# Optimization experiments

Hardware: AMD Instinct MI355X
Metric: run time of the kernel (lower is better)

The kernel has to match this reference:

```python
import jax, jax.numpy as jnp
import numpy as np

N = 25000   # nodes of type 'window'
E = 200000  # edges per relation
H = 512     # hidden_channels
OUT = 250   # out_channels
L = 4       # num_layers
R = 3       # relations: near, close, sim


def setup_inputs() -> dict:
    key = jax.random.key(0)
    ks = jax.random.split(key, 8)
    s = 1.0 / np.sqrt(H).astype(np.float32)
    x = jax.random.normal(ks[0], (N, H), jnp.float32)
    W_pre = jax.random.normal(ks[1], (H, H), jnp.float32) * s
    W_post = jax.random.normal(ks[2], (H, H), jnp.float32) * s
    Wl = jax.random.normal(ks[3], (L, R, H, H), jnp.float32) * s   # SAGEConv lin_l (neighbors)
    Wr = jax.random.normal(ks[4], (L, R, H, H), jnp.float32) * s   # SAGEConv lin_r (root)
    bl = jnp.zeros((L, R, H), jnp.float32)                         # lin_l bias
    W_out = jax.random.normal(ks[5], (H, OUT), jnp.float32) * s
    b_out = jnp.zeros((OUT,), jnp.float32)
    edges = jax.random.randint(ks[6], (R, 2, E), 0, N, jnp.int32)  # [rel, (src,dst), E]
    return dict(x=x, W_pre=W_pre, W_post=W_post, Wl=Wl, Wr=Wr, bl=bl,
                W_out=W_out, b_out=b_out, edges=edges)


def _leaky(v):
    return jnp.where(v >= 0, v, 0.2 * v)


def reference(x, W_pre, W_post, Wl, Wr, bl, W_out, b_out, edges):
    # pretransform + post_transform: leaky(leaky(x @ Wpre) @ Wpost)
    h = _leaky(_leaky(x @ W_pre) @ W_post)

    # per-relation destination in-degree (constant across layers)
    inv_deg = []
    for r in range(R):
        cnt = jax.ops.segment_sum(jnp.ones((E,), h.dtype), edges[r, 1], num_segments=N)
        inv_deg.append(1.0 / jnp.maximum(cnt, 1.0))  # [N]

    for l in range(L):
        acc = jnp.zeros_like(h)
        for r in range(R):
            src, dst = edges[r, 0], edges[r, 1]
            # mean aggregation of neighbor features over destinations
            agg = jax.ops.segment_sum(h[src], dst, num_segments=N) * inv_deg[r][:, None]
            # SAGEConv: lin_l(agg) + lin_r(x_root)
            acc = acc + (agg @ Wl[l, r] + bl[l, r] + h @ Wr[l, r])
        # HeteroConv aggr='mean' across relations, then LeakyReLU(0.2)
        h = _leaky(acc / R)

    return h @ W_out + b_out
```

## Files before the change

kernel.cpp:

```cpp
#include <hip/hip_runtime.h>

#define N_ 25000
#define E_ 200000
#define H_ 512
#define OUT_ 250
#define WSZ (H_ * H_)

typedef unsigned short u16;
typedef unsigned int u32;
typedef __bf16 bf16x8 __attribute__((ext_vector_type(8)));
typedef float f32x4 __attribute__((ext_vector_type(4)));

__device__ __forceinline__ u16 f2b(float f) {
  union { float f; u32 u; } c; c.f = f;
  u32 r = c.u + 0x7FFFu + ((c.u >> 16) & 1u);
  return (u16)(r >> 16);
}
__device__ __forceinline__ void async16(const void* g, void* l) {
  __builtin_amdgcn_global_load_lds((__attribute__((address_space(1))) void*)g,
                                   (__attribute__((address_space(3))) void*)l, 16, 0, 0);
}

__global__ void conv_x(const float* __restrict__ x, u16* __restrict__ xb, int n4) {
  int i = blockIdx.x * 256 + threadIdx.x;
  if (i >= n4) return;
  const float4 v = *(const float4*)(x + (size_t)i * 4);
  ushort4 o;
  o.x = f2b(v.x); o.y = f2b(v.y); o.z = f2b(v.z); o.w = f2b(v.w);
  *(ushort4*)(xb + (size_t)i * 4) = o;
}

__global__ void prep_wt(const float* __restrict__ Wpre, const float* __restrict__ Wpost,
                        const float* __restrict__ Wl, const float* __restrict__ Wr,
                        u16* __restrict__ WT) {
  __shared__ u16 tile[32][33];
  const int id = blockIdx.z;
  const int tx = blockIdx.x, ty = blockIdx.y;
  const int x = threadIdx.x, y = threadIdx.y;
  const float* src = nullptr;
  bool sum3 = false;
  if (id == 0) src = Wpre;
  else if (id == 1) src = Wpost;
  else {
    int li = (id - 2) >> 2, ri = (id - 2) & 3;
    if (ri < 3) src = Wl + (size_t)(li * 3 + ri) * WSZ;
    else { sum3 = true; src = Wr + (size_t)(li * 3) * WSZ; }
  }
#pragma unroll
  for (int i = 0; i < 4; ++i) {
    int row = ty * 32 + y + i * 8;
    int col = tx * 32 + x;
    float f = src[(size_t)row * 512 + col];
    if (sum3) f += src[WSZ + (size_t)row * 512 + col] + src[2 * WSZ + (size_t)row * 512 + col];
    tile[y + i * 8][x] = f2b(f);
  }
  __syncthreads();
#pragma unroll
  for (int i = 0; i < 4; ++i) {
    WT[(size_t)id * WSZ + (tx * 32 + y + i * 8) * 512 + ty * 32 + x] = tile[x][y + i * 8];
  }
}

__global__ void prep_wout(const float* __restrict__ Wout, u16* __restrict__ WoutT) {
  __shared__ u16 tile[32][33];
  const int tx = blockIdx.x, ty = blockIdx.y;
  const int x = threadIdx.x, y = threadIdx.y;
#pragma unroll
  for (int i = 0; i < 4; ++i) {
    int row = ty * 32 + y + i * 8;
    int col = tx * 32 + x;
    tile[y + i * 8][x] = (col < OUT_) ? f2b(Wout[(size_t)row * OUT_ + col]) : (u16)0;
  }
  __syncthreads();
#pragma unroll
  for (int i = 0; i < 4; ++i) {
    WoutT[(tx * 32 + y + i * 8) * 512 + ty * 32 + x] = tile[x][y + i * 8];
  }
}

__global__ void prep_bias(const float* __restrict__ bl, const float* __restrict__ bout,
                          float* __restrict__ blSum, float* __restrict__ bOutF) {
  int t = threadIdx.x;
  for (int l = 0; l < 4; ++l)
    blSum[l * 512 + t] = bl[(l * 3 + 0) * 512 + t] + bl[(l * 3 + 1) * 512 + t] +
                         bl[(l * 3 + 2) * 512 + t];
  if (t < 256) bOutF[t] = (t < OUT_) ? bout[t] : 0.0f;
}

__global__ void hist_kernel(const int* __restrict__ edges, int* __restrict__ counts) {
  int idx = blockIdx.x * 256 + threadIdx.x;
  if (idx >= 3 * E_) return;
  int r = idx / E_, e = idx - r * E_;
  int dst = edges[r * 2 * E_ + E_ + e];
  atomicAdd(&counts[r * N_ + dst], 1);
}

__global__ __launch_bounds__(1024) void scan_kernel(const int* __restrict__ counts,
                                                    int* __restrict__ rowptr,
                                                    int* __restrict__ cursor) {
  const int r = blockIdx.x;
  const int* cnt = counts + r * N_;
  int* rp = rowptr + r * (N_ + 1);
  int* cur = cursor + r * N_;
  __shared__ int wsum[2][16];
  const int tid = threadIdx.x;
  const int wv = tid >> 6, lane = tid & 63;
  int roff = 0;
  int par = 0;
  for (int base = 0; base < N_; base += 1024, par ^= 1) {
    int v = (base + tid < N_) ? cnt[base + tid] : 0;
    int inc = v;
#pragma unroll
    for (int d = 1; d < 64; d <<= 1) {
      int t = __shfl_up(inc, d, 64);
      if (lane >= d) inc += t;
    }
    if (lane == 63) wsum[par][wv] = inc;
    __syncthreads();
    if (tid < 16) {
      int s = wsum[par][tid];
#pragma unroll
      for (int d = 1; d < 16; d <<= 1) {
        int t = __shfl_up(s, d, 64);
        if (tid >= d) s += t;
      }
      wsum[par][tid] = s;
    }
    __syncthreads();
    int woff = (wv == 0) ? 0 : wsum[par][wv - 1];
    int excl = roff + woff + inc - v;
    if (base + tid < N_) { rp[base + tid] = excl; cur[base + tid] = excl; }
    roff += wsum[par][15];
  }
  if (tid == 0) rp[N_] = roff;
}

__global__ void scatter_kernel(const int* __restrict__ edges, int* __restrict__ cursor,
                               int* __restrict__ colidx) {
  int idx = blockIdx.x * 256 + threadIdx.x;
  if (idx >= 3 * E_) return;
  int r = idx / E_, e = idx - r * E_;
  int src = edges[r * 2 * E_ + e];
  int dst = edges[r * 2 * E_ + E_ + e];
  int pos = atomicAdd(&cursor[r * N_ + dst], 1);
  colidx[r * E_ + pos] = src;
}

__global__ void invdeg_kernel(const int* __restrict__ counts, float* __restrict__ invdeg) {
  int idx = blockIdx.x * 256 + threadIdx.x;
  if (idx >= 3 * N_) return;
  invdeg[idx] = 1.0f / fmaxf((float)counts[idx], 1.0f);
}

__device__ __forceinline__ void acc8(float* acc, uint4 u) {
  union { u32 u; float f; } c;
  c.u = u.x << 16;          acc[0] += c.f;
  c.u = u.x & 0xffff0000u;  acc[1] += c.f;
  c.u = u.y << 16;          acc[2] += c.f;
  c.u = u.y & 0xffff0000u;  acc[3] += c.f;
  c.u = u.z << 16;          acc[4] += c.f;
  c.u = u.z & 0xffff0000u;  acc[5] += c.f;
  c.u = u.w << 16;          acc[6] += c.f;
  c.u = u.w & 0xffff0000u;  acc[7] += c.f;
}

__global__ __launch_bounds__(256) void agg_kernel(const u16* __restrict__ h,
                                                  const int* __restrict__ rowptr,
                                                  const int* __restrict__ colidx,
                                                  const float* __restrict__ invdeg,
                                                  u16* __restrict__ agg) {
  const int chunk = blockIdx.x & 7;
  const int nb = blockIdx.x >> 3;
  const int r = blockIdx.y;
  const int wv = threadIdx.x >> 6;
  const int lane = threadIdx.x & 63;
  const int grp = lane >> 3, sub = lane & 7;
  const int node = nb * 32 + wv * 8 + grp;
  if (node >= N_) return;
  const int* rp = rowptr + r * (N_ + 1);
  const int* ci = colidx + r * E_;
  const u16* hb = h + chunk * 64 + sub * 8;
  const int s = rp[node], e = rp[node + 1];
  float acc[8] = {0.f, 0.f, 0.f, 0.f, 0.f, 0.f, 0.f, 0.f};
  int p = s;
  if (p < e) {
    int src = ci[p];
    uint4 u = *(const uint4*)(hb + (size_t)src * 512);
    for (++p; p < e; ++p) {
      int src2 = ci[p];
      uint4 u2 = *(const uint4*)(hb + (size_t)src2 * 512);
      acc8(acc, u);
      u = u2;
    }
    acc8(acc, u);
  }
  const float sc = invdeg[r * N_ + node];
  uint4 o;
  o.x = (u32)f2b(acc[0] * sc) | ((u32)f2b(acc[1] * sc) << 16);
  o.y = (u32)f2b(acc[2] * sc) | ((u32)f2b(acc[3] * sc) << 16);
  o.z = (u32)f2b(acc[4] * sc) | ((u32)f2b(acc[5] * sc) << 16);
  o.w = (u32)f2b(acc[6] * sc) | ((u32)f2b(acc[7] * sc) << 16);
  *(uint4*)(agg + ((size_t)r * N_ + node) * 512 + chunk * 64 + sub * 8) = o;
}

#define BM 128
#define BN 128
#define BK 64
__global__ __launch_bounds__(256, 4) void gemm_mfma(
    const u16* __restrict__ A0, const u16* __restrict__ A1,
    const u16* __restrict__ A2, const u16* __restrict__ A3,
    const u16* __restrict__ Bt, const float* __restrict__ bias,
    u16* __restrict__ C, float* __restrict__ Cf,
    int M, int G, int ldc, int Nreal, float scale, int leaky) {
  __shared__ __align__(16) u16 As[BM * BK];
  __shared__ __align__(16) u16 Bs[BN * BK];
  const int tid = threadIdx.x;
  const int lane = tid & 63;
  const int w = tid >> 6;

  const int gx = gridDim.x;
  const int lin = blockIdx.y * gx + blockIdx.x;
  const int gsz = gx * 8;
  const int grp = lin / gsz;
  const int l = lin - grp * gsz;
  const int rem = (int)gridDim.y - grp * 8;
  int by, bx;
  if (rem >= 8) { by = grp * 8 + (l & 7); bx = l >> 3; }
  else          { by = grp * 8 + l % rem; bx = l / rem; }
  const int row0 = by * BM;
  const int col0 = bx * BN;

  int aOff[4], bOff[4], lOff[4];
#pragma unroll
  for (int i = 0; i < 4; ++i) {
    const int idx = i * 256 + tid;
    const int arow = idx >> 3;
    const int c = (idx & 7) ^ (arow & 7);
    int grow = row0 + arow; if (grow >= M) grow = M - 1;
    aOff[i] = grow * 512 + c * 8;
    bOff[i] = (col0 + arow) * 512 + c * 8;
    lOff[i] = idx * 16;
  }

  const int lm = lane & 15;
  const int lk = lane >> 4;
  const int x0 = ((lk ^ (lane & 7)) << 3);
  const int x1 = (((4 + lk) ^ (lane & 7)) << 3);
  const int wm = (w >> 1) * 64;
  const int wn = (w & 1) * 64;
  int aRow[4], bRow[4];
#pragma unroll
  for (int i = 0; i < 4; ++i) {
    aRow[i] = (wm + i * 16 + lm) * BK;
    bRow[i] = (wn + i * 16 + lm) * BK;
  }

  f32x4 acc[4][4] = {};

  for (int g = 0; g < G; ++g) {
    const u16* Ag = (g == 0) ? A0 : (g == 1) ? A1 : (g == 2) ? A2 : A3;
    const u16* Bg = Bt + ((size_t)g << 18);
#pragma unroll
    for (int ki = 0; ki < 8; ++ki) {
      const u16* Ab = Ag + ki * 64;
      const u16* Bb = Bg + ki * 64;
#pragma unroll
      for (int i = 0; i < 4; ++i) {
        async16(Ab + aOff[i], (char*)As + lOff[i]);
        async16(Bb + bOff[i], (char*)Bs + lOff[i]);
      }
      __syncthreads();
      {
        bf16x8 af[4], bfr[4];
#pragma unroll
        for (int i = 0; i < 4; ++i) {
          af[i]  = *(const bf16x8*)((const char*)As + ((aRow[i] + x0) << 1));
          bfr[i] = *(const bf16x8*)((const char*)Bs + ((bRow[i] + x0) << 1));
        }
#pragma unroll
        for (int i = 0; i < 4; ++i)
#pragma unroll
          for (int j = 0; j < 4; ++j)
            acc[i][j] = __builtin_amdgcn_mfma_f32_16x16x32_bf16(af[i], bfr[j], acc[i][j], 0, 0, 0);
#pragma unroll
        for (int i = 0; i < 4; ++i) {
          af[i]  = *(const bf16x8*)((const char*)As + ((aRow[i] + x1) << 1));
          bfr[i] = *(const bf16x8*)((const char*)Bs + ((bRow[i] + x1) << 1));
        }
#pragma unroll
        for (int i = 0; i < 4; ++i)
#pragma unroll
          for (int j = 0; j < 4; ++j)
            acc[i][j] = __builtin_amdgcn_mfma_f32_16x16x32_bf16(af[i], bfr[j], acc[i][j], 0, 0, 0);
      }
      __syncthreads();
    }
  }

  const int crow_base = row0 + wm + (lk << 2);
  const int ccol_base = col0 + wn + lm;
#pragma unroll
  for (int i = 0; i < 4; ++i) {
#pragma unroll
    for (int j = 0; j < 4; ++j) {
      const int ccol = ccol_base + j * 16;
      const float badd = bias ? bias[ccol] : 0.0f;
#pragma unroll
      for (int rg = 0; rg < 4; ++rg) {
        const int crow = crow_base + i * 16 + rg;
        if (crow < M && ccol < Nreal) {
          float v = (acc[i][j][rg] + badd) * scale;
          if (leaky) v = (v >= 0.0f) ? v : 0.2f * v;
          if (Cf) Cf[(size_t)crow * ldc + ccol] = v;
          else    C[(size_t)crow * ldc + ccol] = f2b(v);
        }
      }
    }
  }
}

extern "C" void kernel_launch(void* const* d_in, const int* in_sizes, int n_in,
                              void* d_out, int out_size, void* d_ws, size_t ws_size,
                              hipStream_t stream) {
  const float* x     = (const float*)d_in[0];
  const float* Wpre  = (const float*)d_in[1];
  const float* Wpost = (const float*)d_in[2];
  const float* Wl    = (const float*)d_in[3];
  const float* Wr    = (const float*)d_in[4];
  const float* bl    = (const float*)d_in[5];
  const float* Wout  = (const float*)d_in[6];
  const float* bout  = (const float*)d_in[7];
  const int*   edges = (const int*)d_in[8];
  float* out = (float*)d_out;

  char* p = (char*)d_ws;
  auto alloc = [&](size_t b) { void* q = (void*)p; p += (b + 255) & ~(size_t)255; return q; };
  u16*   WT     = (u16*)alloc((size_t)18 * WSZ * 2);
  u16*   WoutT  = (u16*)alloc((size_t)256 * 512 * 2);
  float* blSum  = (float*)alloc(4 * 512 * 4);
  float* bOutF  = (float*)alloc(256 * 4);
  u16*   hA     = (u16*)alloc((size_t)N_ * 512 * 2);
  u16*   hB     = (u16*)alloc((size_t)N_ * 512 * 2);
  u16*   aggb   = (u16*)alloc((size_t)3 * N_ * 512 * 2);
  int*   counts = (int*)alloc(3 * N_ * 4);
  float* invdeg = (float*)alloc(3 * N_ * 4);
  int*   rowptr = (int*)alloc(3 * (N_ + 1) * 4);
  int*   cursor = (int*)alloc(3 * N_ * 4);
  int*   colidx = (int*)alloc((size_t)3 * E_ * 4);
  u16*   xb     = aggb;

  hipMemsetAsync(counts, 0, 3 * N_ * 4, stream);
  conv_x<<<(N_ * 512 / 4 + 255) / 256, 256, 0, stream>>>(x, xb, N_ * 512 / 4);
  prep_wt<<<dim3(16, 16, 18), dim3(32, 8), 0, stream>>>(Wpre, Wpost, Wl, Wr, WT);
  prep_wout<<<dim3(8, 16), dim3(32, 8), 0, stream>>>(Wout, WoutT);
  prep_bias<<<1, 512, 0, stream>>>(bl, bout, blSum, bOutF);
  hist_kernel<<<(3 * E_ + 255) / 256, 256, 0, stream>>>(edges, counts);
  scan_kernel<<<3, 1024, 0, stream>>>(counts, rowptr, cursor);
  scatter_kernel<<<(3 * E_ + 255) / 256, 256, 0, stream>>>(edges, cursor, colidx);
  invdeg_kernel<<<(3 * N_ + 255) / 256, 256, 0, stream>>>(counts, invdeg);

  const dim3 blk(256);
  const dim3 g512(512 / 128, (N_ + 127) / 128);
  const dim3 gagg(((N_ + 31) / 32) * 8, 3);
  gemm_mfma<<<g512, blk, 0, stream>>>(xb, xb, xb, xb, WT, nullptr, hA, nullptr,
                                      N_, 1, 512, 512, 1.0f, 1);
  gemm_mfma<<<g512, blk, 0, stream>>>(hA, hA, hA, hA, WT + WSZ, nullptr, hB, nullptr,
                                      N_, 1, 512, 512, 1.0f, 1);

  u16* hc = hB; u16* hn = hA;
  for (int l = 0; l < 4; ++l) {
    agg_kernel<<<gagg, blk, 0, stream>>>(hc, rowptr, colidx, invdeg, aggb);
    gemm_mfma<<<g512, blk, 0, stream>>>(aggb, aggb + (size_t)N_ * 512, aggb + (size_t)2 * N_ * 512, hc,
                                        WT + (size_t)(2 + 4 * l) * WSZ, blSum + l * 512, hn, nullptr,
                                        N_, 4, 512, 512, 1.0f / 3.0f, 1);
    u16* t = hc; hc = hn; hn = t;
  }
  const dim3 gout(256 / 128, (N_ + 127) / 128);
  gemm_mfma<<<gout, blk, 0, stream>>>(hc, hc, hc, hc, WoutT, bOutF, nullptr, out,
                                      N_, 1, OUT_, OUT_, 1.0f, 0);
}
```

Baseline: 867.6 us.

## Register-prefetch GEMM K tiles and fold inverse degree into scan kernel

Replaces the direct global-to-LDS async loads in the MFMA GEMM with a register-staged prefetch. The next K tile is loaded into registers while the current tile is computed, then written to shared memory, so global latency overlaps with MFMA work. Launch bounds drop from 4 to 3 waves-per-EU to make room for the extra registers, at some cost in occupancy. The separate invdeg kernel is folded into the scan kernel to save one launch.

```diff
diff --git a/kernel.cpp b/kernel.cpp
--- a/kernel.cpp
+++ b/kernel.cpp
@@ -15,10 +15,6 @@
   union { float f; u32 u; } c; c.f = f;
   u32 r = c.u + 0x7FFFu + ((c.u >> 16) & 1u);
   return (u16)(r >> 16);
-}
-__device__ __forceinline__ void async16(const void* g, void* l) {
-  __builtin_amdgcn_global_load_lds((__attribute__((address_space(1))) void*)g,
-                                   (__attribute__((address_space(3))) void*)l, 16, 0, 0);
 }
 
 __global__ void conv_x(const float* __restrict__ x, u16* __restrict__ xb, int n4) {
@@ -97,7 +93,8 @@
 
 __global__ __launch_bounds__(1024) void scan_kernel(const int* __restrict__ counts,
                                                     int* __restrict__ rowptr,
-                                                    int* __restrict__ cursor) {
+                                                    int* __restrict__ cursor,
+                                                    float* __restrict__ invdeg) {
   const int r = blockIdx.x;
   const int* cnt = counts + r * N_;
   int* rp = rowptr + r * (N_ + 1);
@@ -129,7 +126,10 @@
     __syncthreads();
     int woff = (wv == 0) ? 0 : wsum[par][wv - 1];
     int excl = roff + woff + inc - v;
-    if (base + tid < N_) { rp[base + tid] = excl; cur[base + tid] = excl; }
+    if (base + tid < N_) {
+      rp[base + tid] = excl; cur[base + tid] = excl;
+      invdeg[r * N_ + base + tid] = 1.0f / fmaxf((float)v, 1.0f);
+    }
     roff += wsum[par][15];
   }
   if (tid == 0) rp[N_] = roff;
@@ -144,12 +144,6 @@
   int dst = edges[r * 2 * E_ + E_ + e];
   int pos = atomicAdd(&cursor[r * N_ + dst], 1);
   colidx[r * E_ + pos] = src;
-}
-
-__global__ void invdeg_kernel(const int* __restrict__ counts, float* __restrict__ invdeg) {
-  int idx = blockIdx.x * 256 + threadIdx.x;
-  if (idx >= 3 * N_) return;
-  invdeg[idx] = 1.0f / fmaxf((float)counts[idx], 1.0f);
 }
 
 __device__ __forceinline__ void acc8(float* acc, uint4 u) {
@@ -206,7 +200,7 @@
 #define BM 128
 #define BN 128
 #define BK 64
-__global__ __launch_bounds__(256, 4) void gemm_mfma(
+__global__ __launch_bounds__(256, 3) void gemm_mfma(
     const u16* __restrict__ A0, const u16* __restrict__ A1,
     const u16* __restrict__ A2, const u16* __restrict__ A3,
     const u16* __restrict__ Bt, const float* __restrict__ bias,
@@ -256,43 +250,60 @@
   }
 
   f32x4 acc[4][4] = {};
-
-  for (int g = 0; g < G; ++g) {
+  uint4 ra[4], rb[4];
+
+  auto gload = [&](int t) {
+    const int g = t >> 3, ki = t & 7;
     const u16* Ag = (g == 0) ? A0 : (g == 1) ? A1 : (g == 2) ? A2 : A3;
-    const u16* Bg = Bt + ((size_t)g << 18);
-#pragma unroll
-    for (int ki = 0; ki < 8; ++ki) {
-      const u16* Ab = Ag + ki * 64;
-      const u16* Bb = Bg + ki * 64;
-#pragma unroll
-      for (int i = 0; i < 4; ++i) {
-        async16(Ab + aOff[i], (char*)As + lOff[i]);
-        async16(Bb + bOff[i], (char*)Bs + lOff[i]);
-      }
-      __syncthreads();
-      {
-        bf16x8 af[4], bfr[4];
-#pragma unroll
-        for (int i = 0; i < 4; ++i) {
-          af[i]  = *(const bf16x8*)((const char*)As + ((aRow[i] + x0) << 1));
-          bfr[i] = *(const bf16x8*)((const char*)Bs + ((bRow[i] + x0) << 1));
-        }
-#pragma unroll
-        for (int i = 0; i < 4; ++i)
-#pragma unroll
-          for (int j = 0; j < 4; ++j)
-            acc[i][j] = __builtin_amdgcn_mfma_f32_16x16x32_bf16(af[i], bfr[j], acc[i][j], 0, 0, 0);
-#pragma unroll
-        for (int i = 0; i < 4; ++i) {
-          af[i]  = *(const bf16x8*)((const char*)As + ((aRow[i] + x1) << 1));
-          bfr[i] = *(const bf16x8*)((const char*)Bs + ((bRow[i] + x1) << 1));
-        }
-#pragma unroll
-        for (int i = 0; i < 4; ++i)
-#pragma unroll
-          for (int j = 0; j < 4; ++j)
-            acc[i][j] = __builtin_amdgcn_mfma_f32_16x16x32_bf16(af[i], bfr[j], acc[i][j], 0, 0, 0);
-      }
+    const u16* Ab = Ag + ki * 64;
+    const u16* Bb = Bt + ((size_t)g << 18) + ki * 64;
+#pragma unroll
+    for (int i = 0; i < 4; ++i) {
+      ra[i] = *(const uint4*)(Ab + aOff[i]);
+      rb[i] = *(const uint4*)(Bb + bOff[i]);
+    }
+  };
+  auto swrite = [&]() {
+#pragma unroll
+    for (int i = 0; i < 4; ++i) {
+      *(uint4*)((char*)As + lOff[i]) = ra[i];
+      *(uint4*)((char*)Bs + lOff[i]) = rb[i];
+    }
+  };
+  auto compute = [&]() {
+    bf16x8 af[4], bfr[4];
+#pragma unroll
+    for (int i = 0; i < 4; ++i) {
+      af[i]  = *(const bf16x8*)((const char*)As + ((aRow[i] + x0) << 1));
+      bfr[i] = *(const bf16x8*)((const char*)Bs + ((bRow[i] + x0) << 1));
+    }
+#pragma unroll
+    for (int i = 0; i < 4; ++i)
+#pragma unroll
+      for (int j = 0; j < 4; ++j)
+        acc[i][j] = __builtin_amdgcn_mfma_f32_16x16x32_bf16(af[i], bfr[j], acc[i][j], 0, 0, 0);
+#pragma unroll
+    for (int i = 0; i < 4; ++i) {
+      af[i]  = *(const bf16x8*)((const char*)As + ((aRow[i] + x1) << 1));
+      bfr[i] = *(const bf16x8*)((const char*)Bs + ((bRow[i] + x1) << 1));
+    }
+#pragma unroll
+    for (int i = 0; i < 4; ++i)
+#pragma unroll
+      for (int j = 0; j < 4; ++j)
+        acc[i][j] = __builtin_amdgcn_mfma_f32_16x16x32_bf16(af[i], bfr[j], acc[i][j], 0, 0, 0);
+  };
+
+  const int T = G << 3;
+  gload(0);
+  swrite();
+  __syncthreads();
+  for (int t = 0; t < T; ++t) {
+    if (t + 1 < T) gload(t + 1);
+    compute();
+    __syncthreads();
+    if (t + 1 < T) {
+      swrite();
       __syncthreads();
     }
   }
@@ -355,12 +366,11 @@
   prep_wout<<<dim3(8, 16), dim3(32, 8), 0, stream>>>(Wout, WoutT);
   prep_bias<<<1, 512, 0, stream>>>(bl, bout, blSum, bOutF);
   hist_kernel<<<(3 * E_ + 255) / 256, 256, 0, stream>>>(edges, counts);
-  scan_kernel<<<3, 1024, 0, stream>>>(counts, rowptr, cursor);
+  scan_kernel<<<3, 1024, 0, stream>>>(counts, rowptr, cursor, invdeg);
   scatter_kernel<<<(3 * E_ + 255) / 256, 256, 0, stream>>>(edges, cursor, colidx);
-  invdeg_kernel<<<(3 * N_ + 255) / 256, 256, 0, stream>>>(counts, invdeg);
 
   const dim3 blk(256);
-  const dim3 g512(512 / 128, (N_ + 127) / 128);
+  const dim3 g512(512 / BN, (N_ + BM - 1) / BM);
   const dim3 gagg(((N_ + 31) / 32) * 8, 3);
   gemm_mfma<<<g512, blk, 0, stream>>>(xb, xb, xb, xb, WT, nullptr, hA, nullptr,
                                       N_, 1, 512, 512, 1.0f, 1);
@@ -375,7 +385,7 @@
                                         N_, 4, 512, 512, 1.0f / 3.0f, 1);
     u16* t = hc; hc = hn; hn = t;
   }
-  const dim3 gout(256 / 128, (N_ + 127) / 128);
+  const dim3 gout(256 / BN, (N_ + BM - 1) / BM);
   gemm_mfma<<<gout, blk, 0, stream>>>(hc, hc, hc, hc, WoutT, bOutF, nullptr, out,
                                       N_, 1, OUT_, OUT_, 1.0f, 0);
 }
```

Result: slower. 2.132 ms (+145.7%).
